# Kernel optimization log

Measured on AMD Instinct MI355X. Metric: run time of the kernel, lower is better.

Reference implementation:

```python
import jax, jax.numpy as jnp
import numpy as np

B, H, CI, O = 8, 16, 16, 16          # batch, child spatial, child caps, parent caps
K, S, ROUTINGS = 3, 1, 3             # kernel, stride, EM iterations
FINAL_LAMBDA = 0.01
EPS = 1e-9


def setup_inputs() -> dict:
    key = jax.random.key(0)
    k1, k2, k3, k4, k5 = jax.random.split(key, 5)
    inputs_pose = jax.random.normal(k1, (B, H, H, CI, 16), dtype=jnp.float32)
    inputs_activation = jax.random.uniform(k2, (B, H, H, CI, 1), dtype=jnp.float32)
    # transformation matrices: [1, k*k*child_caps, parent_caps, 4, 4]
    w = jax.random.normal(k3, (1, K * K * CI, O, 4, 4), dtype=jnp.float32)
    beta_a = jax.random.normal(k4, (O,), dtype=jnp.float32)
    beta_v = jax.random.normal(k5, (O,), dtype=jnp.float32)
    return {"inputs_pose": inputs_pose, "inputs_activation": inputs_activation,
            "w": w, "beta_a": beta_a, "beta_v": beta_v}


def _extract_patches(x, k, s):
    # kernel_tile: im2col-like gather. x: [B, H, W, ...] -> [B, p, p, k, k, ...]
    Hs = x.shape[1]
    p = (Hs - k) // s + 1
    idx = (jnp.arange(p) * s)[:, None] + jnp.arange(k)[None, :]      # [p, k]
    xh = x[:, idx]                   # [B, ph, kh, W, ...]
    patches = xh[:, :, :, idx]       # [B, ph, kh, pw, kw, ...]
    return jnp.swapaxes(patches, 2, 3), p


def _child_index_map(Hs, k, s, p):
    # flat child spatial index feeding each (parent pos, kernel slot)
    ph = np.arange(p)[:, None] * s + np.arange(k)[None, :]           # [p, k]
    ch = ph[:, None, :, None] * Hs + ph[None, :, None, :]            # [p, p, k, k]
    return ch.reshape(p * p, k * k)                                   # [P2, K2]


def reference(inputs_pose, inputs_activation, w, beta_a, beta_v):
    P = (H - K) // S + 1
    P2, K2 = P * P, K * K
    K2CI = K2 * CI

    # ---- kernel_tile ----
    pose_t, _ = _extract_patches(inputs_pose, K, S)       # [B,P,P,K,K,CI,16]
    act_t, _ = _extract_patches(inputs_activation, K, S)  # [B,P,P,K,K,CI,1]
    pose_unroll = pose_t.reshape(B * P2, K2CI, 4, 4)
    act_unroll = act_t.reshape(B * P2, K2CI)

    # ---- compute_votes: tiny 4x4 matmuls per (child slot, parent cap) ----
    votes = jnp.einsum('nkpq,koqr->nkopr', pose_unroll, w[0])  # [B*P2,K2CI,O,4,4]
    votes = votes.reshape(B, P2, K2CI, O, 16)
    act_i = act_unroll.reshape(B, P2, K2CI, 1, 1)

    # ---- spatial routing bookkeeping (static integers) ----
    child_idx = _child_index_map(H, K, S, P)                    # [P2, K2]
    kk_child = np.repeat(child_idx, CI, axis=1)                 # [P2, K2CI]
    counts = np.zeros(H * H, np.float32)
    np.add.at(counts, child_idx.reshape(-1), 1.0)               # parents per child pos
    cap_id = np.tile(np.arange(CI), K2)                         # [K2CI]
    seg = jnp.asarray((kk_child * CI + cap_id[None, :]).reshape(-1))  # [P2*K2CI]
    n_seg = H * H * CI

    # initial routing: uniform over all (parent pos, parent cap) each child feeds
    rr0 = 1.0 / (O * counts[kk_child])                          # [P2, K2CI]
    rr = jnp.asarray(rr0)[None, :, :, None, None]               # bcast [1,P2,K2CI,1,1]

    beta_a_b = beta_a.reshape(1, 1, 1, O, 1)
    beta_v_b = beta_v.reshape(1, 1, 1, O, 1)

    mean = act_j = None
    for it in range(ROUTINGS):
        inv_temp = FINAL_LAMBDA * (1.0 - 0.95 ** (it + 1))
        # ---- M-step: weighted Gaussian statistics ----
        rr_prime = rr * act_i                                   # [B,P2,K2CI,O,1]
        rr_sum = jnp.sum(rr_prime, axis=2, keepdims=True) + EPS # [B,P2,1,O,1]
        mean = jnp.sum(rr_prime * votes, axis=2, keepdims=True) / rr_sum
        var = jnp.sum(rr_prime * jnp.square(votes - mean), axis=2, keepdims=True) / rr_sum + EPS
        cost_h = (beta_v_b + 0.5 * jnp.log(var)) * rr_sum       # [B,P2,1,O,16]
        cost = jnp.sum(cost_h, axis=-1, keepdims=True)          # [B,P2,1,O,1]
        act_j = jax.nn.sigmoid(inv_temp * (beta_a_b - cost))    # [B,P2,1,O,1]
        # ---- E-step: softmax over all (parent pos, parent cap) per child capsule ----
        if it < ROUTINGS - 1:
            log_p = -0.5 * jnp.sum(jnp.square(votes - mean) / var
                                   + jnp.log(2.0 * np.pi * var), axis=-1)  # [B,P2,K2CI,O]
            zz = jnp.log(act_j[..., 0] + EPS) + log_p           # [B,P2,K2CI,O]
            z = jnp.transpose(zz, (1, 2, 0, 3)).reshape(P2 * K2CI, B, O)
            row_max = jnp.max(z, axis=-1)                       # [P2*K2CI, B]
            seg_max = jax.ops.segment_max(row_max, seg, num_segments=n_seg)
            g = seg_max[seg][..., None]
            ez = jnp.exp(z - g)
            denom = jax.ops.segment_sum(jnp.sum(ez, axis=-1), seg, num_segments=n_seg)[seg]
            rr_new = ez / (denom[..., None] + EPS)              # sums to 1 per child capsule
            rr = jnp.transpose(rr_new.reshape(P2, K2CI, B, O), (2, 0, 1, 3))[..., None]

    pose_out = mean[:, :, 0].reshape(B, P, P, O, 16)
    act_out = act_j[:, :, 0].reshape(B, P, P, O, 1)
    return pose_out, act_out
```

## Files before the change

kernel.cpp:

```cpp
#include <hip/hip_runtime.h>

namespace {
constexpr int B_ = 8, H_ = 16, CI_ = 16, O_ = 16, P_ = 14;
constexpr int P2_ = P_ * P_;
constexpr int K2CI_ = 144;
constexpr int NV_ = 2304;
constexpr float EPS_ = 1e-9f;
constexpr float LOG2PI_ = 1.8378770664093453f;

using f2 = __attribute__((ext_vector_type(2))) float;

__device__ __forceinline__ float cnt1(int h) {
  int lo = (h - (P_ - 1)) > 0 ? (h - (P_ - 1)) : 0;
  int hi = h < 2 ? h : 2;
  return (float)(hi - lo + 1);
}

__global__ __launch_bounds__(256) void transpose_all(const float* __restrict__ pose,
                                                     float* __restrict__ pose_t,
                                                     const float* __restrict__ w,
                                                     float* __restrict__ wt) {
  if (blockIdx.x < 2048) {
    const int i = blockIdx.x * 256 + threadIdx.x;
    const int cell = i >> 4, idx = i & 15;
    const int p = idx >> 2, q = idx & 3;
    pose_t[(cell << 4) + (q << 2) + p] = pose[i];
  } else {
    const int i = (blockIdx.x - 2048) * 256 + threadIdx.x;
    const int ko = i >> 4, q = (i >> 2) & 3, r = i & 3;
    wt[(ko << 4) + (r << 2) + q] = w[i];
  }
}

template <int MODE>
__global__ __launch_bounds__(512, 8) void caps_main(
    const float* __restrict__ pose_t, const float* __restrict__ act,
    const float* __restrict__ wt, const float* __restrict__ beta_a,
    const float* __restrict__ beta_v, const float* __restrict__ zin,
    const float* __restrict__ gmax, const float* __restrict__ gden,
    float* __restrict__ zout, float* __restrict__ out) {
  __shared__ float rr_s[(MODE == 0) ? K2CI_ : NV_];
  __shared__ f2 partv[4][512];
  __shared__ float partr[512];
  __shared__ f2 sfin[4][64];
  __shared__ float sfr[64];
  __shared__ float gm_s[(MODE == 0) ? 1 : K2CI_];
  __shared__ float ad_s[(MODE == 0) ? 1 : K2CI_];

  const int tid = threadIdx.x;
  const int wv = __builtin_amdgcn_readfirstlane(tid >> 6);
  const int l = tid & 63;
  const int o = l >> 2, r = l & 3;
  const int pid = blockIdx.x;
  const int b = pid / P2_;
  const int p2 = pid - b * P2_;
  const int pi = p2 / P_;
  const int pj = p2 - pi * P_;
  const float inv_temp = (MODE == 0) ? 0.0005f : (MODE == 1) ? 0.000975f : 0.00142625f;

  if (MODE == 0) {
    if (tid < K2CI_) {
      const int ci = tid & 15, kk = tid >> 4;
      const int ki = (kk >= 6) ? 2 : (kk >= 3) ? 1 : 0, kj = kk - 3 * ki;
      const int cidx = ((b * H_ + pi + ki) * H_ + pj + kj) * CI_ + ci;
      rr_s[tid] = act[cidx] / (16.0f * cnt1(pi + ki) * cnt1(pj + kj));
    }
  } else {
    if (tid < K2CI_) {
      const int ci = tid & 15, kk = tid >> 4;
      const int ki = (kk >= 6) ? 2 : (kk >= 3) ? 1 : 0, kj = kk - 3 * ki;
      const int cidx = ((b * H_ + pi + ki) * H_ + pj + kj) * CI_ + ci;
      gm_s[tid] = gmax[cidx];
      ad_s[tid] = act[cidx] / (gden[cidx] + EPS_);
    }
    __syncthreads();
    for (int i4 = tid; i4 < NV_ / 4; i4 += 512) {
      const float4 z4 = ((const float4*)(zin + (size_t)pid * NV_))[i4];
      const int k = i4 >> 2;
      const float gmk = gm_s[k], adk = ad_s[k];
      float4 r4;
      r4.x = __expf(z4.x - gmk) * adk;
      r4.y = __expf(z4.y - gmk) * adk;
      r4.z = __expf(z4.z - gmk) * adk;
      r4.w = __expf(z4.w - gmk) * adk;
      ((float4*)rr_s)[i4] = r4;
    }
  }
  __syncthreads();

  const float bvo = 16.0f * beta_v[o];
  const float bao = beta_a[o];

  const float* pose_b = pose_t + ((size_t)((b * H_ + pi) * H_ + pj) << 8);
  const float* wt_l = wt + (l << 2);
  const int ci0 = wv * 2;

#define WT_OFF(idx) ((((idx) >> 1) << 12) + ((ci0 + ((idx)&1)) << 8))
#define PB_OFF(idx) (((((idx) >> 1) / 3) << 12) + ((((idx) >> 1) % 3) << 8) + ((ci0 + ((idx)&1)) << 4))

  float prr = 0.f;
  f2 pm01 = {0.f, 0.f}, pm23 = {0.f, 0.f}, pv01 = {0.f, 0.f}, pv23 = {0.f, 0.f};
  {
    float4 wbuf0 = *(const float4*)(wt_l + WT_OFF(0));
    float4 wbuf1 = *(const float4*)(wt_l + WT_OFF(1));
#pragma unroll
    for (int idx = 0; idx < 18; ++idx) {
      const float4 w4 = (idx & 1) ? wbuf1 : wbuf0;
      if (idx < 16) {
        if (idx & 1)
          wbuf1 = *(const float4*)(wt_l + WT_OFF(idx + 2));
        else
          wbuf0 = *(const float4*)(wt_l + WT_OFF(idx + 2));
      }
      const float* pb = pose_b + PB_OFF(idx);
      const float4 P0 = *(const float4*)(pb);
      const float4 P1 = *(const float4*)(pb + 4);
      const float4 P2 = *(const float4*)(pb + 8);
      const float4 P3 = *(const float4*)(pb + 12);
      f2 v01 = (f2){P0.x, P0.y} * w4.x;
      f2 v23 = (f2){P0.z, P0.w} * w4.x;
      v01 = __builtin_elementwise_fma((f2){P1.x, P1.y}, (f2){w4.y, w4.y}, v01);
      v23 = __builtin_elementwise_fma((f2){P1.z, P1.w}, (f2){w4.y, w4.y}, v23);
      v01 = __builtin_elementwise_fma((f2){P2.x, P2.y}, (f2){w4.z, w4.z}, v01);
      v23 = __builtin_elementwise_fma((f2){P2.z, P2.w}, (f2){w4.z, w4.z}, v23);
      v01 = __builtin_elementwise_fma((f2){P3.x, P3.y}, (f2){w4.w, w4.w}, v01);
      v23 = __builtin_elementwise_fma((f2){P3.z, P3.w}, (f2){w4.w, w4.w}, v23);
      const int k = ((idx >> 1) << 4) + ci0 + (idx & 1);
      const float rrk = (MODE == 0) ? rr_s[k] : rr_s[(k << 4) + o];
      prr += rrk;
      const f2 rr2 = {rrk, rrk};
      const f2 a01 = rr2 * v01, a23 = rr2 * v23;
      pm01 += a01;
      pm23 += a23;
      pv01 = __builtin_elementwise_fma(a01, v01, pv01);
      pv23 = __builtin_elementwise_fma(a23, v23, pv23);
    }
  }
  partv[0][tid] = pm01; partv[1][tid] = pm23;
  partv[2][tid] = pv01; partv[3][tid] = pv23;
  partr[tid] = prr;
  __syncthreads();
  if (tid < 320) {
    if (tid < 256) {
      const int st = tid >> 6, li = tid & 63;
      f2 acc = partv[st][li];
#pragma unroll
      for (int wvi = 1; wvi < 8; ++wvi) acc += partv[st][wvi * 64 + li];
      sfin[st][li] = acc;
    } else {
      const int li = tid & 63;
      float acc = partr[li];
#pragma unroll
      for (int wvi = 1; wvi < 8; ++wvi) acc += partr[wvi * 64 + li];
      sfr[li] = acc;
    }
  }
  __syncthreads();
  const f2 S01 = sfin[0][l], S23 = sfin[1][l];
  const f2 V01 = sfin[2][l], V23 = sfin[3][l];
  const float rsum = sfr[l] + EPS_;
  const float irs = 1.0f / rsum;
  const f2 irs2 = {irs, irs};
  const f2 m01 = S01 * irs2, m23 = S23 * irs2;
  const f2 zero2 = {0.f, 0.f}, eps2 = {EPS_, EPS_};
  const f2 va01 = __builtin_elementwise_max(V01 * irs2 - m01 * m01, zero2) + eps2;
  const f2 va23 = __builtin_elementwise_max(V23 * irs2 - m23 * m23, zero2) + eps2;
  float slv = __logf(va01.x) + __logf(va01.y) + __logf(va23.x) + __logf(va23.y);
  slv += __shfl_xor(slv, 1);
  slv += __shfl_xor(slv, 2);
  const float cost = (bvo + 0.5f * slv) * rsum;
  const float aj = 1.0f / (1.0f + __expf(-inv_temp * (bao - cost)));

  if (MODE == 2) {
    if (wv == 0) {
      float* ob = out + ((size_t)(pid * 16 + o) << 4) + r;
      ob[0] = m01.x; ob[4] = m01.y; ob[8] = m23.x; ob[12] = m23.y;
      if (r == 0) out[(size_t)B_ * P2_ * O_ * 16 + pid * 16 + o] = aj;
    }
    return;
  }

  const f2 iv01 = {1.0f / va01.x, 1.0f / va01.y};
  const f2 iv23 = {1.0f / va23.x, 1.0f / va23.y};
  const float Cz = __logf(aj + EPS_) - 0.5f * (slv + 16.0f * LOG2PI_);
  float* zo = zout + (size_t)pid * NV_ + o;
  {
    float4 wbuf0 = *(const float4*)(wt_l + WT_OFF(0));
    float4 wbuf1 = *(const float4*)(wt_l + WT_OFF(1));
#pragma unroll
    for (int idx = 0; idx < 18; ++idx) {
      const float4 w4 = (idx & 1) ? wbuf1 : wbuf0;
      if (idx < 16) {
        if (idx & 1)
          wbuf1 = *(const float4*)(wt_l + WT_OFF(idx + 2));
        else
          wbuf0 = *(const float4*)(wt_l + WT_OFF(idx + 2));
      }
      const float* pb = pose_b + PB_OFF(idx);
      const float4 P0 = *(const float4*)(pb);
      const float4 P1 = *(const float4*)(pb + 4);
      const float4 P2 = *(const float4*)(pb + 8);
      const float4 P3 = *(const float4*)(pb + 12);
      f2 v01 = (f2){P0.x, P0.y} * w4.x;
      f2 v23 = (f2){P0.z, P0.w} * w4.x;
      v01 = __builtin_elementwise_fma((f2){P1.x, P1.y}, (f2){w4.y, w4.y}, v01);
      v23 = __builtin_elementwise_fma((f2){P1.z, P1.w}, (f2){w4.y, w4.y}, v23);
      v01 = __builtin_elementwise_fma((f2){P2.x, P2.y}, (f2){w4.z, w4.z}, v01);
      v23 = __builtin_elementwise_fma((f2){P2.z, P2.w}, (f2){w4.z, w4.z}, v23);
      v01 = __builtin_elementwise_fma((f2){P3.x, P3.y}, (f2){w4.w, w4.w}, v01);
      v23 = __builtin_elementwise_fma((f2){P3.z, P3.w}, (f2){w4.w, w4.w}, v23);
      const f2 d01 = v01 - m01, d23 = v23 - m23;
      const f2 q2 = __builtin_elementwise_fma(d01 * d01, iv01, (d23 * d23) * iv23);
      float q = q2.x + q2.y;
      q += __shfl_xor(q, 1);
      q += __shfl_xor(q, 2);
      const int k = ((idx >> 1) << 4) + ci0 + (idx & 1);
      if (r == 0) zo[k << 4] = Cz - 0.5f * q;
    }
  }
#undef WT_OFF
#undef PB_OFF
}

__global__ __launch_bounds__(256) void seg_reduce(const float* __restrict__ z,
                                                  float* __restrict__ gmax,
                                                  float* __restrict__ gden) {
  const int tid = blockIdx.x * 256 + threadIdx.x;
  const int part = tid & 3, ci = (tid >> 2) & 15, w2 = (tid >> 6) & 15;
  const int h = (tid >> 10) & 15, b = tid >> 14;
  float4 v[9];
  float m = -3.0e38f;
#pragma unroll
  for (int s = 0; s < 9; ++s) {
    const int ki = (s >= 6) ? 2 : (s >= 3) ? 1 : 0, kj = s - 3 * ki;
    const int pi = h - ki, pj = w2 - kj;
    if ((unsigned)pi < (unsigned)P_ && (unsigned)pj < (unsigned)P_) {
      v[s] = *(const float4*)(z + (size_t)(b * P2_ + pi * P_ + pj) * NV_ + s * 256 +
                              ci * 16 + part * 4);
    } else {
      v[s] = make_float4(-3.0e38f, -3.0e38f, -3.0e38f, -3.0e38f);
    }
    m = fmaxf(m, fmaxf(fmaxf(v[s].x, v[s].y), fmaxf(v[s].z, v[s].w)));
  }
  m = fmaxf(m, __shfl_xor(m, 1));
  m = fmaxf(m, __shfl_xor(m, 2));
  float s_ = 0.f;
#pragma unroll
  for (int s = 0; s < 9; ++s) {
    s_ += __expf(v[s].x - m) + __expf(v[s].y - m) + __expf(v[s].z - m) + __expf(v[s].w - m);
  }
  s_ += __shfl_xor(s_, 1);
  s_ += __shfl_xor(s_, 2);
  if (part == 0) {
    gmax[tid >> 2] = m;
    gden[tid >> 2] = s_;
  }
}
}

extern "C" void kernel_launch(void* const* d_in, const int* in_sizes, int n_in,
                              void* d_out, int out_size, void* d_ws, size_t ws_size,
                              hipStream_t stream) {
  const float* pose = (const float*)d_in[0];
  const float* act = (const float*)d_in[1];
  const float* w = (const float*)d_in[2];
  const float* ba = (const float*)d_in[3];
  const float* bv = (const float*)d_in[4];
  float* out = (float*)d_out;

  float* z = (float*)d_ws;
  float* gm = z + (size_t)B_ * P2_ * NV_;
  float* gd = gm + B_ * H_ * H_ * CI_;
  float* wt = gd + B_ * H_ * H_ * CI_;
  float* pt = wt + 36864;

  const int NB = B_ * P2_;
  transpose_all<<<2192, 256, 0, stream>>>(pose, pt, w, wt);
  caps_main<0><<<NB, 512, 0, stream>>>(pt, act, wt, ba, bv, z, gm, gd, z, out);
  seg_reduce<<<512, 256, 0, stream>>>(z, gm, gd);
  caps_main<1><<<NB, 512, 0, stream>>>(pt, act, wt, ba, bv, z, gm, gd, z, out);
  seg_reduce<<<512, 256, 0, stream>>>(z, gm, gd);
  caps_main<2><<<NB, 512, 0, stream>>>(pt, act, wt, ba, bv, z, gm, gd, z, out);
}
```

Measured before the change: 165.1 us.

## Process two parent positions per block to share weight loads

Each caps_main block now handles two consecutive parent positions. Every weight float4 is loaded once and used for the vote computations of both positions, and the grid is halved. The cost targeted is repeated weight traffic and per-block fixed overhead. In exchange the kernel holds more registers and shared memory, and the grid shrinks to 784 blocks, which can lower occupancy. The reduction is serialized over the two positions, adding extra barriers.

```diff
diff --git a/kernel.cpp b/kernel.cpp
--- a/kernel.cpp
+++ b/kernel.cpp
@@ -39,187 +39,213 @@
     const float* __restrict__ beta_v, const float* __restrict__ zin,
     const float* __restrict__ gmax, const float* __restrict__ gden,
     float* __restrict__ zout, float* __restrict__ out) {
-  __shared__ float rr_s[(MODE == 0) ? K2CI_ : NV_];
-  __shared__ f2 partv[4][512];
-  __shared__ float partr[512];
-  __shared__ f2 sfin[4][64];
-  __shared__ float sfr[64];
-  __shared__ float gm_s[(MODE == 0) ? 1 : K2CI_];
-  __shared__ float ad_s[(MODE == 0) ? 1 : K2CI_];
+  constexpr int S = (MODE == 0) ? K2CI_ : NV_;
+  __shared__ float smem[2 * S + 4608 + 576];
+  float* rrA = smem;
+  float* rrB = smem + S;
+  float* comb = smem + 2 * S;
+  f2* partv = (f2*)comb;
+  float* partr = comb + 4096;
+  f2* sfin = (f2*)(comb + 4608);
+  float* sfr = comb + 4608 + 512;
 
   const int tid = threadIdx.x;
   const int wv = __builtin_amdgcn_readfirstlane(tid >> 6);
   const int l = tid & 63;
   const int o = l >> 2, r = l & 3;
-  const int pid = blockIdx.x;
-  const int b = pid / P2_;
-  const int p2 = pid - b * P2_;
-  const int pi = p2 / P_;
-  const int pj = p2 - pi * P_;
+  const int pid0 = blockIdx.x * 2;
+  const int bA = pid0 / P2_, p2A = pid0 - bA * P2_;
+  const int piA = p2A / P_, pjA = p2A - piA * P_;
+  const int pid1 = pid0 + 1;
+  const int bB = pid1 / P2_, p2B = pid1 - bB * P2_;
+  const int piB = p2B / P_, pjB = p2B - piB * P_;
   const float inv_temp = (MODE == 0) ? 0.0005f : (MODE == 1) ? 0.000975f : 0.00142625f;
 
   if (MODE == 0) {
-    if (tid < K2CI_) {
-      const int ci = tid & 15, kk = tid >> 4;
+    if (tid < 288) {
+      const int pp = tid >= 144;
+      const int idx = pp ? tid - 144 : tid;
+      const int ci = idx & 15, kk = idx >> 4;
       const int ki = (kk >= 6) ? 2 : (kk >= 3) ? 1 : 0, kj = kk - 3 * ki;
+      const int b = pp ? bB : bA, pi = pp ? piB : piA, pj = pp ? pjB : pjA;
       const int cidx = ((b * H_ + pi + ki) * H_ + pj + kj) * CI_ + ci;
-      rr_s[tid] = act[cidx] / (16.0f * cnt1(pi + ki) * cnt1(pj + kj));
+      (pp ? rrB : rrA)[idx] = act[cidx] / (16.0f * cnt1(pi + ki) * cnt1(pj + kj));
     }
   } else {
-    if (tid < K2CI_) {
-      const int ci = tid & 15, kk = tid >> 4;
+    if (tid < 288) {
+      const int pp = tid >= 144;
+      const int idx = pp ? tid - 144 : tid;
+      const int ci = idx & 15, kk = idx >> 4;
       const int ki = (kk >= 6) ? 2 : (kk >= 3) ? 1 : 0, kj = kk - 3 * ki;
+      const int b = pp ? bB : bA, pi = pp ? piB : piA, pj = pp ? pjB : pjA;
       const int cidx = ((b * H_ + pi + ki) * H_ + pj + kj) * CI_ + ci;
-      gm_s[tid] = gmax[cidx];
-      ad_s[tid] = act[cidx] / (gden[cidx] + EPS_);
+      comb[pp * 288 + idx] = gmax[cidx];
+      comb[pp * 288 + 144 + idx] = act[cidx] / (gden[cidx] + EPS_);
     }
     __syncthreads();
-    for (int i4 = tid; i4 < NV_ / 4; i4 += 512) {
-      const float4 z4 = ((const float4*)(zin + (size_t)pid * NV_))[i4];
+    for (int t = tid; t < 1152; t += 512) {
+      const int pp = t >= 576;
+      const int i4 = pp ? t - 576 : t;
+      const float4 z4 = ((const float4*)(zin + (size_t)(pid0 + pp) * NV_))[i4];
       const int k = i4 >> 2;
-      const float gmk = gm_s[k], adk = ad_s[k];
+      const float gmk = comb[pp * 288 + k], adk = comb[pp * 288 + 144 + k];
       float4 r4;
       r4.x = __expf(z4.x - gmk) * adk;
       r4.y = __expf(z4.y - gmk) * adk;
       r4.z = __expf(z4.z - gmk) * adk;
       r4.w = __expf(z4.w - gmk) * adk;
-      ((float4*)rr_s)[i4] = r4;
+      ((float4*)(pp ? rrB : rrA))[i4] = r4;
     }
   }
   __syncthreads();
 
   const float bvo = 16.0f * beta_v[o];
   const float bao = beta_a[o];
-
-  const float* pose_b = pose_t + ((size_t)((b * H_ + pi) * H_ + pj) << 8);
-  const float* wt_l = wt + (l << 2);
   const int ci0 = wv * 2;
 
-#define WT_OFF(idx) ((((idx) >> 1) << 12) + ((ci0 + ((idx)&1)) << 8))
-#define PB_OFF(idx) (((((idx) >> 1) / 3) << 12) + ((((idx) >> 1) % 3) << 8) + ((ci0 + ((idx)&1)) << 4))
-
-  float prr = 0.f;
-  f2 pm01 = {0.f, 0.f}, pm23 = {0.f, 0.f}, pv01 = {0.f, 0.f}, pv23 = {0.f, 0.f};
-  {
-    float4 wbuf0 = *(const float4*)(wt_l + WT_OFF(0));
-    float4 wbuf1 = *(const float4*)(wt_l + WT_OFF(1));
-#pragma unroll
-    for (int idx = 0; idx < 18; ++idx) {
-      const float4 w4 = (idx & 1) ? wbuf1 : wbuf0;
-      if (idx < 16) {
-        if (idx & 1)
-          wbuf1 = *(const float4*)(wt_l + WT_OFF(idx + 2));
-        else
-          wbuf0 = *(const float4*)(wt_l + WT_OFF(idx + 2));
-      }
-      const float* pb = pose_b + PB_OFF(idx);
-      const float4 P0 = *(const float4*)(pb);
-      const float4 P1 = *(const float4*)(pb + 4);
-      const float4 P2 = *(const float4*)(pb + 8);
-      const float4 P3 = *(const float4*)(pb + 12);
-      f2 v01 = (f2){P0.x, P0.y} * w4.x;
-      f2 v23 = (f2){P0.z, P0.w} * w4.x;
-      v01 = __builtin_elementwise_fma((f2){P1.x, P1.y}, (f2){w4.y, w4.y}, v01);
-      v23 = __builtin_elementwise_fma((f2){P1.z, P1.w}, (f2){w4.y, w4.y}, v23);
-      v01 = __builtin_elementwise_fma((f2){P2.x, P2.y}, (f2){w4.z, w4.z}, v01);
-      v23 = __builtin_elementwise_fma((f2){P2.z, P2.w}, (f2){w4.z, w4.z}, v23);
-      v01 = __builtin_elementwise_fma((f2){P3.x, P3.y}, (f2){w4.w, w4.w}, v01);
-      v23 = __builtin_elementwise_fma((f2){P3.z, P3.w}, (f2){w4.w, w4.w}, v23);
-      const int k = ((idx >> 1) << 4) + ci0 + (idx & 1);
-      const float rrk = (MODE == 0) ? rr_s[k] : rr_s[(k << 4) + o];
-      prr += rrk;
+  const float* wtw = wt + (l << 2) + (ci0 << 8);
+  const float* pbA = pose_t + ((size_t)((bA * H_ + piA) * H_ + pjA) << 8) + (ci0 << 4);
+  const float* pbB = pose_t + ((size_t)((bB * H_ + piB) * H_ + pjB) << 8) + (ci0 << 4);
+  const int rb1 = (ci0 << 4) + o;
+#define WT_OFF(idx) ((((idx) >> 1) << 12) + (((idx)&1) << 8))
+#define PB_OFF(idx) (((((idx) >> 1) / 3) << 12) + ((((idx) >> 1) % 3) << 8) + (((idx)&1) << 4))
+#define RR_OFF0(idx) ((((idx) >> 1) << 4) + ((idx)&1))
+#define RR_OFF1(idx) ((((idx) >> 1) << 8) + (((idx)&1) << 4))
+
+#define VOTE(pb, w4, v01, v23)                                              \
+  {                                                                         \
+    const float4 P0 = *(const float4*)(pb);                                 \
+    const float4 P1 = *(const float4*)((pb) + 4);                           \
+    const float4 P2 = *(const float4*)((pb) + 8);                           \
+    const float4 P3 = *(const float4*)((pb) + 12);                          \
+    v01 = (f2){P0.x, P0.y} * (w4).x;                                        \
+    v23 = (f2){P0.z, P0.w} * (w4).x;                                        \
+    v01 = __builtin_elementwise_fma((f2){P1.x, P1.y}, (f2){(w4).y, (w4).y}, v01); \
+    v23 = __builtin_elementwise_fma((f2){P1.z, P1.w}, (f2){(w4).y, (w4).y}, v23); \
+    v01 = __builtin_elementwise_fma((f2){P2.x, P2.y}, (f2){(w4).z, (w4).z}, v01); \
+    v23 = __builtin_elementwise_fma((f2){P2.z, P2.w}, (f2){(w4).z, (w4).z}, v23); \
+    v01 = __builtin_elementwise_fma((f2){P3.x, P3.y}, (f2){(w4).w, (w4).w}, v01); \
+    v23 = __builtin_elementwise_fma((f2){P3.z, P3.w}, (f2){(w4).w, (w4).w}, v23); \
+  }
+
+  float prrA = 0.f, prrB = 0.f;
+  const f2 zz = {0.f, 0.f};
+  f2 pm01A = zz, pm23A = zz, pv01A = zz, pv23A = zz;
+  f2 pm01B = zz, pm23B = zz, pv01B = zz, pv23B = zz;
+#pragma unroll
+  for (int idx = 0; idx < 18; ++idx) {
+    const float4 w4 = *(const float4*)(wtw + WT_OFF(idx));
+    f2 v01, v23;
+    VOTE(pbA + PB_OFF(idx), w4, v01, v23);
+    {
+      const float rrk = (MODE == 0) ? rrA[ci0 + RR_OFF0(idx)] : rrA[rb1 + RR_OFF1(idx)];
+      prrA += rrk;
       const f2 rr2 = {rrk, rrk};
       const f2 a01 = rr2 * v01, a23 = rr2 * v23;
-      pm01 += a01;
-      pm23 += a23;
-      pv01 = __builtin_elementwise_fma(a01, v01, pv01);
-      pv23 = __builtin_elementwise_fma(a23, v23, pv23);
-    }
-  }
-  partv[0][tid] = pm01; partv[1][tid] = pm23;
-  partv[2][tid] = pv01; partv[3][tid] = pv23;
-  partr[tid] = prr;
-  __syncthreads();
-  if (tid < 320) {
-    if (tid < 256) {
-      const int st = tid >> 6, li = tid & 63;
-      f2 acc = partv[st][li];
-#pragma unroll
-      for (int wvi = 1; wvi < 8; ++wvi) acc += partv[st][wvi * 64 + li];
-      sfin[st][li] = acc;
-    } else {
-      const int li = tid & 63;
-      float acc = partr[li];
-#pragma unroll
-      for (int wvi = 1; wvi < 8; ++wvi) acc += partr[wvi * 64 + li];
-      sfr[li] = acc;
-    }
-  }
-  __syncthreads();
-  const f2 S01 = sfin[0][l], S23 = sfin[1][l];
-  const f2 V01 = sfin[2][l], V23 = sfin[3][l];
-  const float rsum = sfr[l] + EPS_;
-  const float irs = 1.0f / rsum;
-  const f2 irs2 = {irs, irs};
-  const f2 m01 = S01 * irs2, m23 = S23 * irs2;
-  const f2 zero2 = {0.f, 0.f}, eps2 = {EPS_, EPS_};
-  const f2 va01 = __builtin_elementwise_max(V01 * irs2 - m01 * m01, zero2) + eps2;
-  const f2 va23 = __builtin_elementwise_max(V23 * irs2 - m23 * m23, zero2) + eps2;
-  float slv = __logf(va01.x) + __logf(va01.y) + __logf(va23.x) + __logf(va23.y);
-  slv += __shfl_xor(slv, 1);
-  slv += __shfl_xor(slv, 2);
-  const float cost = (bvo + 0.5f * slv) * rsum;
-  const float aj = 1.0f / (1.0f + __expf(-inv_temp * (bao - cost)));
+      pm01A += a01; pm23A += a23;
+      pv01A = __builtin_elementwise_fma(a01, v01, pv01A);
+      pv23A = __builtin_elementwise_fma(a23, v23, pv23A);
+    }
+    VOTE(pbB + PB_OFF(idx), w4, v01, v23);
+    {
+      const float rrk = (MODE == 0) ? rrB[ci0 + RR_OFF0(idx)] : rrB[rb1 + RR_OFF1(idx)];
+      prrB += rrk;
+      const f2 rr2 = {rrk, rrk};
+      const f2 a01 = rr2 * v01, a23 = rr2 * v23;
+      pm01B += a01; pm23B += a23;
+      pv01B = __builtin_elementwise_fma(a01, v01, pv01B);
+      pv23B = __builtin_elementwise_fma(a23, v23, pv23B);
+    }
+  }
+
+  f2 m01[2], m23[2], va01[2], va23[2];
+  float rsum[2], slvv[2], ajv[2];
+#pragma unroll
+  for (int pp = 0; pp < 2; ++pp) {
+    partv[0 * 512 + tid] = pp ? pm01B : pm01A;
+    partv[1 * 512 + tid] = pp ? pm23B : pm23A;
+    partv[2 * 512 + tid] = pp ? pv01B : pv01A;
+    partv[3 * 512 + tid] = pp ? pv23B : pv23A;
+    partr[tid] = pp ? prrB : prrA;
+    __syncthreads();
+    if (tid < 320) {
+      if (tid < 256) {
+        const int st = tid >> 6, li = tid & 63;
+        f2 acc = partv[st * 512 + li];
+#pragma unroll
+        for (int wvi = 1; wvi < 8; ++wvi) acc += partv[st * 512 + wvi * 64 + li];
+        sfin[st * 64 + li] = acc;
+      } else {
+        const int li = tid & 63;
+        float acc = partr[li];
+#pragma unroll
+        for (int wvi = 1; wvi < 8; ++wvi) acc += partr[wvi * 64 + li];
+        sfr[li] = acc;
+      }
+    }
+    __syncthreads();
+    const f2 S01 = sfin[0 * 64 + l], S23 = sfin[1 * 64 + l];
+    const f2 V01 = sfin[2 * 64 + l], V23 = sfin[3 * 64 + l];
+    const float rs = sfr[l] + EPS_;
+    const float irs = 1.0f / rs;
+    const f2 irs2 = {irs, irs};
+    const f2 mm01 = S01 * irs2, mm23 = S23 * irs2;
+    const f2 eps2 = {EPS_, EPS_};
+    const f2 vv01 = __builtin_elementwise_max(V01 * irs2 - mm01 * mm01, zz) + eps2;
+    const f2 vv23 = __builtin_elementwise_max(V23 * irs2 - mm23 * mm23, zz) + eps2;
+    float slv = __logf(vv01.x) + __logf(vv01.y) + __logf(vv23.x) + __logf(vv23.y);
+    slv += __shfl_xor(slv, 1);
+    slv += __shfl_xor(slv, 2);
+    const float cost = (bvo + 0.5f * slv) * rs;
+    const float aj = 1.0f / (1.0f + __expf(-inv_temp * (bao - cost)));
+    m01[pp] = mm01; m23[pp] = mm23; va01[pp] = vv01; va23[pp] = vv23;
+    rsum[pp] = rs; slvv[pp] = slv; ajv[pp] = aj;
+    if (pp == 0) __syncthreads();
+  }
 
   if (MODE == 2) {
-    if (wv == 0) {
-      float* ob = out + ((size_t)(pid * 16 + o) << 4) + r;
-      ob[0] = m01.x; ob[4] = m01.y; ob[8] = m23.x; ob[12] = m23.y;
-      if (r == 0) out[(size_t)B_ * P2_ * O_ * 16 + pid * 16 + o] = aj;
+    if (wv < 2) {
+      const int pp = wv;
+      float* ob = out + ((size_t)((pid0 + pp) * 16 + o) << 4) + r;
+      ob[0] = m01[pp].x; ob[4] = m01[pp].y; ob[8] = m23[pp].x; ob[12] = m23[pp].y;
+      if (r == 0) out[(size_t)B_ * P2_ * O_ * 16 + (pid0 + pp) * 16 + o] = ajv[pp];
     }
     return;
   }
 
-  const f2 iv01 = {1.0f / va01.x, 1.0f / va01.y};
-  const f2 iv23 = {1.0f / va23.x, 1.0f / va23.y};
-  const float Cz = __logf(aj + EPS_) - 0.5f * (slv + 16.0f * LOG2PI_);
-  float* zo = zout + (size_t)pid * NV_ + o;
-  {
-    float4 wbuf0 = *(const float4*)(wt_l + WT_OFF(0));
-    float4 wbuf1 = *(const float4*)(wt_l + WT_OFF(1));
-#pragma unroll
-    for (int idx = 0; idx < 18; ++idx) {
-      const float4 w4 = (idx & 1) ? wbuf1 : wbuf0;
-      if (idx < 16) {
-        if (idx & 1)
-          wbuf1 = *(const float4*)(wt_l + WT_OFF(idx + 2));
-        else
-          wbuf0 = *(const float4*)(wt_l + WT_OFF(idx + 2));
-      }
-      const float* pb = pose_b + PB_OFF(idx);
-      const float4 P0 = *(const float4*)(pb);
-      const float4 P1 = *(const float4*)(pb + 4);
-      const float4 P2 = *(const float4*)(pb + 8);
-      const float4 P3 = *(const float4*)(pb + 12);
-      f2 v01 = (f2){P0.x, P0.y} * w4.x;
-      f2 v23 = (f2){P0.z, P0.w} * w4.x;
-      v01 = __builtin_elementwise_fma((f2){P1.x, P1.y}, (f2){w4.y, w4.y}, v01);
-      v23 = __builtin_elementwise_fma((f2){P1.z, P1.w}, (f2){w4.y, w4.y}, v23);
-      v01 = __builtin_elementwise_fma((f2){P2.x, P2.y}, (f2){w4.z, w4.z}, v01);
-      v23 = __builtin_elementwise_fma((f2){P2.z, P2.w}, (f2){w4.z, w4.z}, v23);
-      v01 = __builtin_elementwise_fma((f2){P3.x, P3.y}, (f2){w4.w, w4.w}, v01);
-      v23 = __builtin_elementwise_fma((f2){P3.z, P3.w}, (f2){w4.w, w4.w}, v23);
-      const f2 d01 = v01 - m01, d23 = v23 - m23;
-      const f2 q2 = __builtin_elementwise_fma(d01 * d01, iv01, (d23 * d23) * iv23);
-      float q = q2.x + q2.y;
-      q += __shfl_xor(q, 1);
-      q += __shfl_xor(q, 2);
-      const int k = ((idx >> 1) << 4) + ci0 + (idx & 1);
-      if (r == 0) zo[k << 4] = Cz - 0.5f * q;
+  const f2 iv01A = {1.0f / va01[0].x, 1.0f / va01[0].y};
+  const f2 iv23A = {1.0f / va23[0].x, 1.0f / va23[0].y};
+  const f2 iv01B = {1.0f / va01[1].x, 1.0f / va01[1].y};
+  const f2 iv23B = {1.0f / va23[1].x, 1.0f / va23[1].y};
+  const float CzA = __logf(ajv[0] + EPS_) - 0.5f * (slvv[0] + 16.0f * LOG2PI_);
+  const float CzB = __logf(ajv[1] + EPS_) - 0.5f * (slvv[1] + 16.0f * LOG2PI_);
+  float* zoA = zout + (size_t)pid0 * NV_ + (ci0 << 4) + o;
+  float* zoB = zoA + NV_;
+#pragma unroll
+  for (int idx = 0; idx < 18; ++idx) {
+    const float4 w4 = *(const float4*)(wtw + WT_OFF(idx));
+    f2 vA01, vA23, vB01, vB23;
+    VOTE(pbA + PB_OFF(idx), w4, vA01, vA23);
+    VOTE(pbB + PB_OFF(idx), w4, vB01, vB23);
+    const f2 dA01 = vA01 - m01[0], dA23 = vA23 - m23[0];
+    const f2 dB01 = vB01 - m01[1], dB23 = vB23 - m23[1];
+    const f2 qa2 = __builtin_elementwise_fma(dA01 * dA01, iv01A, (dA23 * dA23) * iv23A);
+    const f2 qb2 = __builtin_elementwise_fma(dB01 * dB01, iv01B, (dB23 * dB23) * iv23B);
+    float qa = qa2.x + qa2.y, qb = qb2.x + qb2.y;
+    qa += __shfl_xor(qa, 1);
+    qb += __shfl_xor(qb, 1);
+    qa += __shfl_xor(qa, 2);
+    qb += __shfl_xor(qb, 2);
+    if (r == 0) {
+      zoA[RR_OFF1(idx)] = CzA - 0.5f * qa;
+      zoB[RR_OFF1(idx)] = CzB - 0.5f * qb;
     }
   }
 #undef WT_OFF
 #undef PB_OFF
+#undef RR_OFF0
+#undef RR_OFF1
+#undef VOTE
 }
 
 __global__ __launch_bounds__(256) void seg_reduce(const float* __restrict__ z,
@@ -274,7 +300,7 @@
   float* wt = gd + B_ * H_ * H_ * CI_;
   float* pt = wt + 36864;
 
-  const int NB = B_ * P2_;
+  const int NB = B_ * P2_ / 2;
   transpose_all<<<2192, 256, 0, stream>>>(pose, pt, w, wt);
   caps_main<0><<<NB, 512, 0, stream>>>(pt, act, wt, ba, bv, z, gm, gd, z, out);
   seg_reduce<<<512, 256, 0, stream>>>(z, gm, gd);
```

After: 250.3 us. 51.6% more time.
